# Kernel tuning notes

Hardware: AMD Instinct MI355X
Metric: run time of the kernel (lower is better)

Reference implementation:

```python
import jax, jax.numpy as jnp
import numpy as np

F = 128; K = 64; SR_CUT = 10.0
NB = 5; NRI = 3; NRA = 2; NRO = 1
N_ATOMS = 10000; N_PAIRS = 320000


def act(x):
    # shifted softplus: softplus(x) - log(2)
    return jax.nn.softplus(x) - jnp.log(2.0).astype(x.dtype)


def residual(x, W1, b1, W2, b2):
    # PhysNet residual: x + dense2(dense1(act(x))) with activation on dense1
    h = act(act(x) @ W1 + b1)
    return x + h @ W2 + b2


def cutoff_fn(D):
    x = D / SR_CUT
    x3 = x * x * x; x4 = x3 * x; x5 = x4 * x
    return jnp.where(x < 1.0, 1.0 - 6.0 * x5 + 15.0 * x4 - 10.0 * x3, 0.0)


def setup_inputs() -> dict:
    key = jax.random.key(0)
    ks = jax.random.split(key, 24)

    def nrm(k, shape, s=0.05):
        return (jax.random.normal(k, shape) * s).astype(jnp.float32)

    inp = {}
    inp["Z"] = jax.random.randint(ks[0], (N_ATOMS,), 1, 95)
    inp["R"] = (jax.random.normal(ks[1], (N_ATOMS, 3)) * 3.0).astype(jnp.float32)
    inp["idx_i"] = jax.random.randint(ks[2], (N_PAIRS,), 0, N_ATOMS)
    inp["idx_j"] = jax.random.randint(ks[3], (N_PAIRS,), 0, N_ATOMS)
    s3 = float(np.sqrt(3.0))
    inp["embeddings"] = jax.random.uniform(ks[4], (95, F), minval=-s3, maxval=s3).astype(jnp.float32)
    inp["rbf_centers"] = jnp.linspace(1.0, float(np.exp(-SR_CUT)), K).astype(jnp.float32)
    width = (0.5 / ((1.0 - float(np.exp(-SR_CUT))) / K)) ** 2
    inp["rbf_widths"] = jnp.full((K,), width, dtype=jnp.float32)
    inp["k2f_W"] = nrm(ks[5], (NB, K, F))
    inp["Wi"] = nrm(ks[6], (NB, F, F)); inp["bi"] = jnp.zeros((NB, F), jnp.float32)
    inp["Wj"] = nrm(ks[7], (NB, F, F)); inp["bj"] = jnp.zeros((NB, F), jnp.float32)
    inp["ri_W1"] = nrm(ks[8], (NB, NRI, F, F)); inp["ri_b1"] = jnp.zeros((NB, NRI, F), jnp.float32)
    inp["ri_W2"] = nrm(ks[9], (NB, NRI, F, F)); inp["ri_b2"] = jnp.zeros((NB, NRI, F), jnp.float32)
    inp["dW"] = nrm(ks[10], (NB, F, F)); inp["db"] = jnp.zeros((NB, F), jnp.float32)
    inp["u"] = jnp.ones((NB, F), jnp.float32)
    inp["ra_W1"] = nrm(ks[11], (NB, NRA, F, F)); inp["ra_b1"] = jnp.zeros((NB, NRA, F), jnp.float32)
    inp["ra_W2"] = nrm(ks[12], (NB, NRA, F, F)); inp["ra_b2"] = jnp.zeros((NB, NRA, F), jnp.float32)
    inp["ro_W1"] = nrm(ks[13], (NB, NRO, F, F)); inp["ro_b1"] = jnp.zeros((NB, NRO, F), jnp.float32)
    inp["ro_W2"] = nrm(ks[14], (NB, NRO, F, F)); inp["ro_b2"] = jnp.zeros((NB, NRO, F), jnp.float32)
    inp["out_W"] = nrm(ks[15], (NB, F, 2))
    inp["Escale"] = jnp.ones((95,), jnp.float32); inp["Eshift"] = jnp.zeros((95,), jnp.float32)
    inp["Qscale"] = jnp.ones((95,), jnp.float32); inp["Qshift"] = jnp.zeros((95,), jnp.float32)
    return inp


def reference(Z, R, idx_i, idx_j, embeddings, rbf_centers, rbf_widths, k2f_W, Wi, bi, Wj, bj,
              ri_W1, ri_b1, ri_W2, ri_b2, dW, db, u, ra_W1, ra_b1, ra_W2, ra_b2,
              ro_W1, ro_b1, ro_W2, ro_b2, out_W, Escale, Eshift, Qscale, Qshift):
    N = R.shape[0]
    # gather-based interatomic distances: gather -> sub -> sumsq -> relu -> sqrt
    dR = R[idx_i] - R[idx_j]                                   # [P,3]
    Dij = jnp.sqrt(jax.nn.relu(jnp.sum(dR * dR, axis=-1)))     # [P]
    # RBF expansion with smooth cutoff
    rbf = cutoff_fn(Dij)[:, None] * jnp.exp(-rbf_widths * (jnp.exp(-Dij)[:, None] - rbf_centers) ** 2)  # [P,K]
    x = embeddings[Z]                                          # [N,F]
    Ea = jnp.zeros((N,), x.dtype)
    Qa = jnp.zeros((N,), x.dtype)
    nhloss = jnp.zeros((), x.dtype)
    last2 = None
    for b in range(NB):
        # --- interaction layer ---
        g = rbf @ k2f_W[b]                                     # [P,F]
        xa = act(x)
        xi = act(xa @ Wi[b] + bi[b])                           # [N,F]
        xj_feat = act(xa @ Wj[b] + bj[b])                      # [N,F]
        msg = g * xj_feat[idx_j]                               # [P,F] gather + modulate
        m = xi + jax.ops.segment_sum(msg, idx_i, num_segments=N)
        for l in range(NRI):
            m = residual(m, ri_W1[b, l], ri_b1[b, l], ri_W2[b, l], ri_b2[b, l])
        m = act(m)
        x = u[b] * x + m @ dW[b] + db[b]
        for l in range(NRA):
            x = residual(x, ra_W1[b, l], ra_b1[b, l], ra_W2[b, l], ra_b2[b, l])
        # --- output block ---
        o = x
        for l in range(NRO):
            o = residual(o, ro_W1[b, l], ro_b1[b, l], ro_W2[b, l], ro_b2[b, l])
        out = act(o) @ out_W[b]                                # [N,2] -> (Ea, Qa)
        Ea = Ea + out[:, 0]
        Qa = Qa + out[:, 1]
        out2 = out * out
        if b > 0:
            nhloss = nhloss + jnp.mean(out2 / (out2 + last2 + 1e-7))
        last2 = out2
    Ea = Escale[Z] * Ea + Eshift[Z]
    Qa = Qscale[Z] * Qa + Qshift[Z]
    return Ea, Qa, Dij, nhloss
```

## Files before the change

### kernel.cpp

```cpp
#include <hip/hip_runtime.h>

typedef __attribute__((ext_vector_type(8))) short bfrag;
typedef __attribute__((ext_vector_type(4))) float ffrag;

__device__ __forceinline__ unsigned short f2b(float f){
  unsigned int u = __float_as_uint(f);
  return (unsigned short)((u + 0x7FFFu + ((u >> 16) & 1u)) >> 16);
}
__device__ __forceinline__ float b2f_lo(unsigned int v){
  return __uint_as_float(v << 16);
}
__device__ __forceinline__ float b2f_hi(unsigned int v){
  return __uint_as_float(v & 0xFFFF0000u);
}
__device__ __forceinline__ int rfl(int v){ return __builtin_amdgcn_readfirstlane(v); }
__device__ __forceinline__ float actf(float v){
  float e = __builtin_amdgcn_exp2f(-fabsf(v)*1.44269504088896341f);
  return fmaxf(v, 0.f) + __builtin_amdgcn_logf(1.f + e)*0.69314718055994531f - 0.69314718055994531f;
}

__global__ __launch_bounds__(256) void k_zero(float* p, int n){
  int i = blockIdx.x*256 + threadIdx.x;
  if (i < n) p[i] = 0.f;
}

__global__ __launch_bounds__(256) void k_dij_count(
    const float* __restrict__ R, const int* __restrict__ idx_i, const int* __restrict__ idx_j,
    float* __restrict__ DijF, float* __restrict__ Dout, int* __restrict__ counts, int P){
  int p = blockIdx.x*256 + threadIdx.x;
  if (p >= P) return;
  int i = idx_i[p], j = idx_j[p];
  float dx = R[i*3+0] - R[j*3+0];
  float dy = R[i*3+1] - R[j*3+1];
  float dz = R[i*3+2] - R[j*3+2];
  float D = sqrtf(fmaxf(dx*dx + dy*dy + dz*dz, 0.f));
  DijF[p] = D;
  Dout[p] = D;
  atomicAdd(&counts[i], 1);
}

__global__ __launch_bounds__(1024) void k_scan(const int* __restrict__ counts,
    int* __restrict__ cursor, int N){
  __shared__ int wsum[16];
  int tid = threadIdx.x;
  int CH = (N + 1023) >> 10;
  int base = tid * CH;
  int s = 0;
  for (int i = 0; i < CH; ++i){
    int idx = base + i;
    s += (idx < N) ? counts[idx] : 0;
  }
  int lane = tid & 63, w = tid >> 6;
  int v = s;
  #pragma unroll
  for (int off = 1; off < 64; off <<= 1){
    int t = __shfl_up(v, off, 64);
    if (lane >= off) v += t;
  }
  if (lane == 63) wsum[w] = v;
  __syncthreads();
  if (tid < 16){
    int t = wsum[tid];
    int vv = t;
    #pragma unroll
    for (int off = 1; off < 16; off <<= 1){
      int u = __shfl_up(vv, off, 64);
      if (tid >= off) vv += u;
    }
    wsum[tid] = vv - t;
  }
  __syncthreads();
  int run = (v - s) + wsum[w];
  for (int i = 0; i < CH; ++i){
    int idx = base + i;
    if (idx < N){ cursor[idx] = run; run += counts[idx]; }
  }
}

__global__ __launch_bounds__(256) void k_scatter(const int* __restrict__ idx_i,
    const int* __restrict__ idx_j, const float* __restrict__ DijF,
    int* __restrict__ cursor, int* __restrict__ i_s, int* __restrict__ j_s,
    float* __restrict__ D_s, int P){
  int p = blockIdx.x*256 + threadIdx.x;
  if (p >= P) return;
  int i = idx_i[p];
  int pos = atomicAdd(&cursor[i], 1);
  i_s[pos] = i;
  j_s[pos] = idx_j[p];
  D_s[pos] = DijF[p];
}

__global__ __launch_bounds__(256) void k_prep2(
    const float* __restrict__ D_s, const float* __restrict__ cent, const float* __restrict__ wid,
    unsigned short* __restrict__ rbf_s,
    const float* __restrict__ riW1, const float* __restrict__ riW2,
    const float* __restrict__ dW,   const float* __restrict__ raW1,
    const float* __restrict__ raW2, const float* __restrict__ roW1,
    const float* __restrict__ roW2, const float* __restrict__ Wi,
    const float* __restrict__ Wj,   const float* __restrict__ k2f,
    const float* __restrict__ outW,
    unsigned short* __restrict__ WBall, unsigned short* __restrict__ k2fP,
    unsigned short* __restrict__ outWB, int P){
  int gid0 = blockIdx.x*256 + threadIdx.x;
  if (gid0 < P*8){
    int t = gid0 >> 3, kg = gid0 & 7;
    float D = D_s[t];
    float xc = D * 0.1f;
    float cut = 0.f;
    if (xc < 1.f){
      float x3 = xc*xc*xc, x4 = x3*xc, x5 = x4*xc;
      cut = 1.f - 6.f*x5 + 15.f*x4 - 10.f*x3;
    }
    float eD = __builtin_amdgcn_exp2f(-D*1.44269504088896341f);
    bfrag o;
    #pragma unroll
    for (int i = 0; i < 8; ++i){
      int k = kg*8 + i;
      float tt = eD - cent[k];
      float v = cut * __builtin_amdgcn_exp2f(-wid[k]*tt*tt*1.44269504088896341f);
      o[i] = (short)f2b(v);
    }
    *(bfrag*)(rbf_s + (size_t)gid0*8) = o;
    return;
  }
  int gid = gid0 - P*8;
  if (gid < 75*2048){
    int i = gid >> 11, r = gid & 2047;
    const float* S;
    int slot;
    if (i < 15)      { S = riW1 + (size_t)i*16384;      slot = (i/3)*15 + 2*(i%3); }
    else if (i < 30) { int j=i-15; S = riW2 + (size_t)j*16384; slot = (j/3)*15 + 2*(j%3) + 1; }
    else if (i < 35) { int j=i-30; S = dW   + (size_t)j*16384; slot = j*15 + 6; }
    else if (i < 45) { int j=i-35; S = raW1 + (size_t)j*16384; slot = (j/2)*15 + 7 + 2*(j%2); }
    else if (i < 55) { int j=i-45; S = raW2 + (size_t)j*16384; slot = (j/2)*15 + 8 + 2*(j%2); }
    else if (i < 60) { int j=i-55; S = roW1 + (size_t)j*16384; slot = j*15 + 11; }
    else if (i < 65) { int j=i-60; S = roW2 + (size_t)j*16384; slot = j*15 + 12; }
    else if (i < 70) { int j=i-65; S = Wi   + (size_t)j*16384; slot = ((j==0)?4:(j-1))*15 + 13; }
    else             { int j=i-70; S = Wj   + (size_t)j*16384; slot = ((j==0)?4:(j-1))*15 + 14; }
    int fr = r >> 6, l = r & 63;
    int T = fr >> 2, k0 = fr & 3;
    int n = T*16 + (l & 15);
    int kbase = k0*32 + (l >> 4)*8;
    unsigned short* D = WBall + ((size_t)slot*2048 + r)*8;
    ushort4 o0, o1;
    o0.x=f2b(S[(kbase+0)*128+n]); o0.y=f2b(S[(kbase+1)*128+n]);
    o0.z=f2b(S[(kbase+2)*128+n]); o0.w=f2b(S[(kbase+3)*128+n]);
    o1.x=f2b(S[(kbase+4)*128+n]); o1.y=f2b(S[(kbase+5)*128+n]);
    o1.z=f2b(S[(kbase+6)*128+n]); o1.w=f2b(S[(kbase+7)*128+n]);
    ((ushort4*)D)[0]=o0; ((ushort4*)D)[1]=o1;
  } else if (gid < 75*2048 + 5120){
    int g = gid - 75*2048;
    int l = g & 63, fr = (g >> 6) & 15, b = g >> 10;
    int tile = fr >> 1, kh = fr & 1;
    const float* src = k2f + (size_t)b*64*128;
    int n = tile*16 + (l & 15);
    int kbase = kh*32 + (l >> 4)*8;
    ushort4 o0, o1;
    o0.x = f2b(src[(kbase+0)*128+n]); o0.y = f2b(src[(kbase+1)*128+n]);
    o0.z = f2b(src[(kbase+2)*128+n]); o0.w = f2b(src[(kbase+3)*128+n]);
    o1.x = f2b(src[(kbase+4)*128+n]); o1.y = f2b(src[(kbase+5)*128+n]);
    o1.z = f2b(src[(kbase+6)*128+n]); o1.w = f2b(src[(kbase+7)*128+n]);
    ushort4* dst = (ushort4*)(k2fP + (size_t)g*8);
    dst[0] = o0; dst[1] = o1;
  } else if (gid < 75*2048 + 5120 + 1280){
    int g = gid - (75*2048 + 5120);
    int b = g >> 8, r = g & 255;
    int l = r & 63;
    int col = l & 15;
    int k0 = r >> 6;
    int kbase = k0*32 + (l >> 4)*8;
    ushort4 o0 = {0,0,0,0}, o1 = {0,0,0,0};
    if (col < 2){
      const float* S = outW + (size_t)b*256;
      o0.x=f2b(S[(kbase+0)*2+col]); o0.y=f2b(S[(kbase+1)*2+col]);
      o0.z=f2b(S[(kbase+2)*2+col]); o0.w=f2b(S[(kbase+3)*2+col]);
      o1.x=f2b(S[(kbase+4)*2+col]); o1.y=f2b(S[(kbase+5)*2+col]);
      o1.z=f2b(S[(kbase+6)*2+col]); o1.w=f2b(S[(kbase+7)*2+col]);
    }
    unsigned short* D = outWB + ((size_t)b*256 + r)*8;
    ((ushort4*)D)[0]=o0; ((ushort4*)D)[1]=o1;
  }
}

__device__ __forceinline__ void mmtile(const unsigned short* tile,
    const unsigned short* __restrict__ WB, int w, int l, ffrag C[4]){
  int m = l & 15, q = l >> 4;
  bfrag A[4];
  #pragma unroll
  for (int k0 = 0; k0 < 4; ++k0)
    A[k0] = *(const bfrag*)(tile + m*136 + k0*32 + q*8);
  #pragma unroll
  for (int tt = 0; tt < 4; ++tt){
    ffrag c = {0.f,0.f,0.f,0.f};
    const bfrag* bp = (const bfrag*)(WB + (((w*4+tt)*4)*64 + l)*8);
    #pragma unroll
    for (int k0 = 0; k0 < 4; ++k0)
      c = __builtin_amdgcn_mfma_f32_16x16x32_bf16(A[k0], bp[k0*64], c, 0, 0, 0);
    C[tt] = c;
  }
}

__global__ __launch_bounds__(128) void k_phase1m(
    const int* __restrict__ Z, const float* __restrict__ emb,
    const unsigned short* __restrict__ WB45,
    const float* __restrict__ bi0, const float* __restrict__ bj0,
    float* __restrict__ x_g, float* __restrict__ m_g, unsigned short* __restrict__ xjb_g, int N){
  __shared__ unsigned short tile[16*136];
  int tid = threadIdx.x, w = tid >> 6, l = tid & 63;
  int m = l & 15, q = l >> 4, rbase = blockIdx.x*16;
  #pragma unroll
  for (int r = 0; r < 4; ++r){
    int row = rbase + q*4 + r;
    int z = Z[row];
    #pragma unroll
    for (int tt = 0; tt < 4; ++tt){
      int c = (w*4+tt)*16 + m;
      float v = emb[(size_t)z*128 + c];
      x_g[(size_t)row*128 + c] = v;
      tile[(q*4+r)*136 + c] = f2b(actf(v));
    }
  }
  __syncthreads();
  ffrag C[4];
  mmtile(tile, WB45 + 13*16384, w, l, C);
  #pragma unroll
  for (int tt = 0; tt < 4; ++tt){
    int c = (w*4+tt)*16 + m;
    float bb = bi0[c];
    #pragma unroll
    for (int r = 0; r < 4; ++r)
      m_g[(size_t)(rbase + q*4 + r)*128 + c] = actf(C[tt][r] + bb);
  }
  mmtile(tile, WB45 + 14*16384, w, l, C);
  #pragma unroll
  for (int tt = 0; tt < 4; ++tt){
    int c = (w*4+tt)*16 + m;
    float bb = bj0[c];
    #pragma unroll
    for (int r = 0; r < 4; ++r)
      xjb_g[(size_t)(rbase + q*4 + r)*128 + c] = f2b(actf(C[tt][r] + bb));
  }
}

__global__ __launch_bounds__(256, 4) void k_pairmsg2(
    const unsigned short* __restrict__ rbf_s, const unsigned short* __restrict__ k2fP,
    const int* __restrict__ i_s, const int* __restrict__ j_s,
    const unsigned short* __restrict__ xj, float* __restrict__ m_g, int P){
  __shared__ float G[4][16*130];
  int tid = threadIdx.x, w = tid >> 6, l = tid & 63;
  float* Gw = &G[w][0];
  bfrag B[16];
  #pragma unroll
  for (int t = 0; t < 16; ++t)
    B[t] = *(const bfrag*)(k2fP + (size_t)(t*64 + l)*8);
  int wstart = (blockIdx.x*4 + w)*64;
  if (wstart >= P) return;
  int row16 = l & 15, quad = l >> 4;
  float a0 = 0.f, a1 = 0.f;
  int iCur = -1;
  #pragma unroll 1
  for (int bi2 = 0; bi2 < 4; ++bi2){
    int bt = wstart + bi2*16;
    bfrag A0 = *(const bfrag*)(rbf_s + (size_t)(bt + row16)*64 + quad*8);
    bfrag A1 = *(const bfrag*)(rbf_s + (size_t)(bt + row16)*64 + 32 + quad*8);
    int ip[16], jp[16];
    #pragma unroll
    for (int g = 0; g < 4; ++g){
      int4 it = *(const int4*)(i_s + bt + g*4);
      int4 jt = *(const int4*)(j_s + bt + g*4);
      ip[g*4+0]=rfl(it.x); ip[g*4+1]=rfl(it.y); ip[g*4+2]=rfl(it.z); ip[g*4+3]=rfl(it.w);
      jp[g*4+0]=rfl(jt.x); jp[g*4+1]=rfl(jt.y); jp[g*4+2]=rfl(jt.z); jp[g*4+3]=rfl(jt.w);
    }
    unsigned int xv[16];
    #pragma unroll
    for (int k = 0; k < 16; ++k)
      xv[k] = *(const unsigned int*)(xj + (size_t)jp[k]*128 + 2*l);
    #pragma unroll
    for (int t = 0; t < 8; ++t){
      ffrag C = {0.f,0.f,0.f,0.f};
      C = __builtin_amdgcn_mfma_f32_16x16x32_bf16(A0, B[t*2],   C, 0, 0, 0);
      C = __builtin_amdgcn_mfma_f32_16x16x32_bf16(A1, B[t*2+1], C, 0, 0, 0);
      #pragma unroll
      for (int r = 0; r < 4; ++r)
        Gw[(quad*4+r)*130 + t*16 + row16] = C[r];
    }
    #pragma unroll
    for (int k = 0; k < 16; ++k){
      int i = ip[k];
      if (i != iCur){
        if (iCur >= 0){
          unsafeAtomicAdd(&m_g[(size_t)iCur*128 + 2*l],     a0);
          unsafeAtomicAdd(&m_g[(size_t)iCur*128 + 2*l + 1], a1);
        }
        iCur = i; a0 = 0.f; a1 = 0.f;
      }
      float g0 = Gw[k*130 + 2*l], g1 = Gw[k*130 + 2*l + 1];
      a0 = fmaf(g0, b2f_lo(xv[k]), a0);
      a1 = fmaf(g1, b2f_hi(xv[k]), a1);
    }
  }
  if (iCur >= 0){
    unsafeAtomicAdd(&m_g[(size_t)iCur*128 + 2*l],     a0);
    unsafeAtomicAdd(&m_g[(size_t)iCur*128 + 2*l + 1], a1);
  }
}

template<int HASNEXT, int NH>
__global__ __launch_bounds__(512, 6) void k_phase2m(
    float* __restrict__ m_g, float* __restrict__ x_g, unsigned short* __restrict__ xjb_g,
    const unsigned short* __restrict__ WBb,
    const float* __restrict__ rib1, const float* __restrict__ rib2,
    const float* __restrict__ db, const float* __restrict__ u,
    const float* __restrict__ rab1, const float* __restrict__ rab2,
    const float* __restrict__ rob1, const float* __restrict__ rob2,
    const float* __restrict__ biN, const float* __restrict__ bjN,
    const unsigned short* __restrict__ outWBb,
    float* __restrict__ Ea, float* __restrict__ Qa,
    float* __restrict__ last2, float* __restrict__ nh, int N){
  __shared__ unsigned short tiles[2][16*136];
  __shared__ float biasS[16*128];
  int tid = threadIdx.x, w = tid >> 6, l = tid & 63;
  int m = l & 15, q = l >> 4, rbase = blockIdx.x*16;
  int c = w*16 + m;
  ffrag mC, xC, C;
  float xrow[4];
  int cur = 0;
  const int nst = HASNEXT ? 15 : 13;
  const int slotSeq[15] = {0,1,2,3,4,5,6,7,8,9,10,
                           HASNEXT?13:11, HASNEXT?14:12, 11, 12};
  bfrag Bb[2][4];
  #pragma unroll
  for (int k0 = 0; k0 < 4; ++k0)
    Bb[0][k0] = *(const bfrag*)(WBb + (size_t)slotSeq[0]*16384 + (size_t)((w*4+k0)*64 + l)*8);

  if (tid < 128){
    biasS[0*128+tid]  = rib1[tid];
    biasS[1*128+tid]  = rib1[128+tid];
    biasS[2*128+tid]  = rib1[256+tid];
    biasS[3*128+tid]  = rib2[tid];
    biasS[4*128+tid]  = rib2[128+tid];
    biasS[5*128+tid]  = rib2[256+tid];
    biasS[6*128+tid]  = db[tid];
    biasS[7*128+tid]  = u[tid];
    biasS[8*128+tid]  = rab1[tid];
    biasS[9*128+tid]  = rab1[128+tid];
    biasS[10*128+tid] = rab2[tid];
    biasS[11*128+tid] = rab2[128+tid];
    biasS[12*128+tid] = rob1[tid];
    biasS[13*128+tid] = rob2[tid];
    biasS[14*128+tid] = biN[tid];
    biasS[15*128+tid] = bjN[tid];
  }
  #pragma unroll
  for (int r = 0; r < 4; ++r){
    int row = rbase + q*4 + r;
    xrow[r] = x_g[(size_t)row*128 + c];
    float v = m_g[(size_t)row*128 + c];
    mC[r] = v;
    tiles[0][(q*4+r)*136 + c] = f2b(actf(v));
  }
  #pragma unroll 2
  for (int s = 0; s < nst; ++s){
    __syncthreads();
    if (s+1 < nst){
      #pragma unroll
      for (int k0 = 0; k0 < 4; ++k0)
        Bb[(s+1)&1][k0] = *(const bfrag*)(WBb + (size_t)slotSeq[s+1]*16384 + (size_t)((w*4+k0)*64 + l)*8);
    }
    {
      const unsigned short* tp = &tiles[cur][0];
      ffrag cc = {0.f,0.f,0.f,0.f};
      #pragma unroll
      for (int k0 = 0; k0 < 4; ++k0){
        bfrag A = *(const bfrag*)(tp + m*136 + k0*32 + q*8);
        cc = __builtin_amdgcn_mfma_f32_16x16x32_bf16(A, Bb[s&1][k0], cc, 0, 0, 0);
      }
      C = cc;
    }
    if (HASNEXT && s == 11){
      float bb = biasS[14*128 + c];
      #pragma unroll
      for (int r = 0; r < 4; ++r)
        m_g[(size_t)(rbase + q*4 + r)*128 + c] = actf(C[r] + bb);
    } else if (HASNEXT && s == 12){
      float bb = biasS[15*128 + c];
      #pragma unroll
      for (int r = 0; r < 4; ++r)
        xjb_g[(size_t)(rbase + q*4 + r)*128 + c] = f2b(actf(C[r] + bb));
    } else if (s == 6){
      float uu = biasS[7*128 + c], bb = biasS[6*128 + c];
      #pragma unroll
      for (int r = 0; r < 4; ++r){
        float nv = uu*xrow[r] + C[r] + bb;
        xC[r] = nv;
        tiles[1-cur][(q*4+r)*136 + c] = f2b(actf(nv));
      }
      cur ^= 1;
    } else if (s == 1 || s == 3 || s == 5){
      float bb = biasS[(3 + (s>>1))*128 + c];
      #pragma unroll
      for (int r = 0; r < 4; ++r){
        float nv = mC[r] + C[r] + bb;
        mC[r] = nv;
        tiles[1-cur][(q*4+r)*136 + c] = f2b(actf(nv));
      }
      cur ^= 1;
    } else if (s == 8 || s == 10){
      float bb = biasS[(10 + ((s-8)>>1))*128 + c];
      #pragma unroll
      for (int r = 0; r < 4; ++r){
        float nv = xC[r] + C[r] + bb;
        xC[r] = nv;
        tiles[1-cur][(q*4+r)*136 + c] = f2b(actf(nv));
        if (HASNEXT && s == 10)
          x_g[(size_t)(rbase + q*4 + r)*128 + c] = nv;
      }
      cur ^= 1;
    } else if ((HASNEXT && s == 14) || (!HASNEXT && s == 12)){
      float bb = biasS[13*128 + c];
      #pragma unroll
      for (int r = 0; r < 4; ++r){
        float ov = xC[r] + C[r] + bb;
        tiles[1-cur][(q*4+r)*136 + c] = f2b(actf(ov));
      }
      cur ^= 1;
    } else {
      int bidx = (s==0)?0:(s==2)?1:(s==4)?2:(s==7)?8:(s==9)?9:12;
      float bb = biasS[bidx*128 + c];
      #pragma unroll
      for (int r = 0; r < 4; ++r)
        tiles[1-cur][(q*4+r)*136 + c] = f2b(actf(C[r] + bb));
      cur ^= 1;
    }
  }
  __syncthreads();
  if (w == 0){
    const unsigned short* tp = &tiles[cur][0];
    bfrag A[4];
    #pragma unroll
    for (int k0 = 0; k0 < 4; ++k0)
      A[k0] = *(const bfrag*)(tp + m*136 + k0*32 + q*8);
    ffrag Ch = {0.f,0.f,0.f,0.f};
    #pragma unroll
    for (int k0 = 0; k0 < 4; ++k0){
      bfrag B = *(const bfrag*)(outWBb + (size_t)(k0*64 + l)*8);
      Ch = __builtin_amdgcn_mfma_f32_16x16x32_bf16(A[k0], B, Ch, 0, 0, 0);
    }
    int col = m;
    if (col < 2){
      float tpa = 0.f;
      #pragma unroll
      for (int r = 0; r < 4; ++r){
        int row = rbase + q*4 + r;
        float val = Ch[r];
        if (NH){
          if (col == 0) Ea[row] += val; else Qa[row] += val;
        } else {
          if (col == 0) Ea[row]  = val; else Qa[row]  = val;
        }
        float sq = val*val;
        if (NH){
          float lastv = last2[row*2 + col];
          tpa += sq/(sq + lastv + 1e-7f);
        }
        last2[row*2 + col] = sq;
      }
      if (NH) unsafeAtomicAdd(nh, tpa);
    }
  }
}

__global__ __launch_bounds__(256) void k_final(
    const int* __restrict__ Z, const float* __restrict__ Ea, const float* __restrict__ Qa,
    const float* __restrict__ Es, const float* __restrict__ Eh,
    const float* __restrict__ Qs, const float* __restrict__ Qh,
    const float* __restrict__ nh, float* __restrict__ out, int N, int P){
  int n = blockIdx.x*256 + threadIdx.x;
  if (n < N){
    int z = Z[n];
    out[n]   = Es[z]*Ea[n] + Eh[z];
    out[N+n] = Qs[z]*Qa[n] + Qh[z];
  }
  if (blockIdx.x == 0 && threadIdx.x == 0)
    out[(size_t)2*N + P] = nh[0] / (2.f * (float)N);
}

extern "C" void kernel_launch(void* const* d_in, const int* in_sizes, int n_in,
                              void* d_out, int out_size, void* d_ws, size_t ws_size,
                              hipStream_t stream){
  const int N = in_sizes[0];
  const int P = in_sizes[2];
  const int F = 128;

  const int* Z      = (const int*)d_in[0];
  const float* R    = (const float*)d_in[1];
  const int* idx_i  = (const int*)d_in[2];
  const int* idx_j  = (const int*)d_in[3];
  const float* emb  = (const float*)d_in[4];
  const float* cent = (const float*)d_in[5];
  const float* wid  = (const float*)d_in[6];
  const float* k2f  = (const float*)d_in[7];
  const float* Wi   = (const float*)d_in[8];  const float* bi   = (const float*)d_in[9];
  const float* Wj   = (const float*)d_in[10]; const float* bj   = (const float*)d_in[11];
  const float* riW1 = (const float*)d_in[12]; const float* rib1 = (const float*)d_in[13];
  const float* riW2 = (const float*)d_in[14]; const float* rib2 = (const float*)d_in[15];
  const float* dWp  = (const float*)d_in[16]; const float* dbp  = (const float*)d_in[17];
  const float* u    = (const float*)d_in[18];
  const float* raW1 = (const float*)d_in[19]; const float* rab1 = (const float*)d_in[20];
  const float* raW2 = (const float*)d_in[21]; const float* rab2 = (const float*)d_in[22];
  const float* roW1 = (const float*)d_in[23]; const float* rob1 = (const float*)d_in[24];
  const float* roW2 = (const float*)d_in[25]; const float* rob2 = (const float*)d_in[26];
  const float* outW = (const float*)d_in[27];
  const float* Es   = (const float*)d_in[28]; const float* Eh   = (const float*)d_in[29];
  const float* Qs   = (const float*)d_in[30]; const float* Qh   = (const float*)d_in[31];

  char* ws = (char*)d_ws;
  size_t off = 0;
  float* DijF  = (float*)(ws + off); off += (size_t)P*4;
  float* D_s   = (float*)(ws + off); off += (size_t)P*4;
  int*   i_s   = (int*)  (ws + off); off += (size_t)P*4;
  int*   j_s   = (int*)  (ws + off); off += (size_t)P*4;
  unsigned short* rbf_s = (unsigned short*)(ws + off); off += (size_t)P*64*2;
  unsigned short* k2fP  = (unsigned short*)(ws + off); off += (size_t)5*16*64*8*2;
  unsigned short* WBall = (unsigned short*)(ws + off); off += (size_t)75*16384*2;
  unsigned short* outWB = (unsigned short*)(ws + off); off += (size_t)5*2048*2;
  float* x     = (float*)(ws + off); off += (size_t)N*F*4;
  unsigned short* xjb = (unsigned short*)(ws + off); off += (size_t)N*F*2;
  float* m     = (float*)(ws + off); off += (size_t)N*F*4;
  float* last2 = (float*)(ws + off); off += (size_t)N*2*4;
  float* Ea    = (float*)(ws + off); off += (size_t)N*4;
  float* Qa    = (float*)(ws + off); off += (size_t)N*4;
  float* nh    = (float*)(ws + off); off += 256;
  int*   counts= (int*)  (ws + off); off += (size_t)N*4;
  int*   cursor= (int*)  (ws + off); off += (size_t)N*4;

  float* outF = (float*)d_out;
  float* Dout = outF + (size_t)2*N;

  const int nzero = N + 64;
  k_zero<<<dim3((nzero+255)/256), dim3(256), 0, stream>>>(nh, nzero);
  k_dij_count<<<dim3((P+255)/256), dim3(256), 0, stream>>>(R, idx_i, idx_j, DijF, Dout, counts, P);
  k_scan<<<dim3(1), dim3(1024), 0, stream>>>(counts, cursor, N);
  k_scatter<<<dim3((P+255)/256), dim3(256), 0, stream>>>(idx_i, idx_j, DijF, cursor, i_s, j_s, D_s, P);
  const int prep2n = P*8 + 75*2048 + 5120 + 1280;
  k_prep2<<<dim3((prep2n+255)/256), dim3(256), 0, stream>>>(
      D_s, cent, wid, rbf_s,
      riW1, riW2, dWp, raW1, raW2, roW1, roW2, Wi, Wj, k2f, outW,
      WBall, k2fP, outWB, P);

  const int G16 = (N + 15)/16;
  k_phase1m<<<dim3(G16), dim3(128), 0, stream>>>(Z, emb, WBall + (size_t)4*15*16384,
                                                 bi, bj, x, m, xjb, N);

  const int pmg = (P + 255)/256;
  for (int b = 0; b < 5; ++b){
    k_pairmsg2<<<dim3(pmg), dim3(256), 0, stream>>>(rbf_s, k2fP + (size_t)b*16*64*8,
                                                    i_s, j_s, xjb, m, P);
    const unsigned short* WBb = WBall + (size_t)b*15*16384;
    const float* a_rib1 = rib1 + (size_t)b*3*F;
    const float* a_rib2 = rib2 + (size_t)b*3*F;
    const float* a_db   = dbp  + (size_t)b*F;
    const float* a_u    = u    + (size_t)b*F;
    const float* a_rab1 = rab1 + (size_t)b*2*F;
    const float* a_rab2 = rab2 + (size_t)b*2*F;
    const float* a_rob1 = rob1 + (size_t)b*F;
    const float* a_rob2 = rob2 + (size_t)b*F;
    int bn = (b < 4) ? (b+1) : 0;
    const float* a_biN = bi + (size_t)bn*F;
    const float* a_bjN = bj + (size_t)bn*F;
    const unsigned short* oWB = outWB + (size_t)b*2048;
    if (b == 0){
      k_phase2m<1,0><<<dim3(G16), dim3(512), 0, stream>>>(m, x, xjb, WBb,
        a_rib1, a_rib2, a_db, a_u, a_rab1, a_rab2, a_rob1, a_rob2,
        a_biN, a_bjN, oWB, Ea, Qa, last2, nh, N);
    } else if (b < 4){
      k_phase2m<1,1><<<dim3(G16), dim3(512), 0, stream>>>(m, x, xjb, WBb,
        a_rib1, a_rib2, a_db, a_u, a_rab1, a_rab2, a_rob1, a_rob2,
        a_biN, a_bjN, oWB, Ea, Qa, last2, nh, N);
    } else {
      k_phase2m<0,1><<<dim3(G16), dim3(512), 0, stream>>>(m, x, xjb, WBb,
        a_rib1, a_rib2, a_db, a_u, a_rab1, a_rab2, a_rob1, a_rob2,
        a_biN, a_bjN, oWB, Ea, Qa, last2, nh, N);
    }
  }
  k_final<<<dim3((N+255)/256), dim3(256), 0, stream>>>(Z, Ea, Qa, Es, Eh, Qs, Qh, nh, outF, N, P);
}
```

Before: 424.5 us.

## Fuse pair message aggregation into per-atom block kernel with LDS accumulation

```diff
diff --git a/kernel.cpp b/kernel.cpp
--- a/kernel.cpp
+++ b/kernel.cpp
@@ -242,72 +242,13 @@
   }
 }
 
-__global__ __launch_bounds__(256, 4) void k_pairmsg2(
+template<int HASNEXT, int NH>
+__global__ __launch_bounds__(512, 4) void k_block2(
     const unsigned short* __restrict__ rbf_s, const unsigned short* __restrict__ k2fP,
     const int* __restrict__ i_s, const int* __restrict__ j_s,
-    const unsigned short* __restrict__ xj, float* __restrict__ m_g, int P){
-  __shared__ float G[4][16*130];
-  int tid = threadIdx.x, w = tid >> 6, l = tid & 63;
-  float* Gw = &G[w][0];
-  bfrag B[16];
-  #pragma unroll
-  for (int t = 0; t < 16; ++t)
-    B[t] = *(const bfrag*)(k2fP + (size_t)(t*64 + l)*8);
-  int wstart = (blockIdx.x*4 + w)*64;
-  if (wstart >= P) return;
-  int row16 = l & 15, quad = l >> 4;
-  float a0 = 0.f, a1 = 0.f;
-  int iCur = -1;
-  #pragma unroll 1
-  for (int bi2 = 0; bi2 < 4; ++bi2){
-    int bt = wstart + bi2*16;
-    bfrag A0 = *(const bfrag*)(rbf_s + (size_t)(bt + row16)*64 + quad*8);
-    bfrag A1 = *(const bfrag*)(rbf_s + (size_t)(bt + row16)*64 + 32 + quad*8);
-    int ip[16], jp[16];
-    #pragma unroll
-    for (int g = 0; g < 4; ++g){
-      int4 it = *(const int4*)(i_s + bt + g*4);
-      int4 jt = *(const int4*)(j_s + bt + g*4);
-      ip[g*4+0]=rfl(it.x); ip[g*4+1]=rfl(it.y); ip[g*4+2]=rfl(it.z); ip[g*4+3]=rfl(it.w);
-      jp[g*4+0]=rfl(jt.x); jp[g*4+1]=rfl(jt.y); jp[g*4+2]=rfl(jt.z); jp[g*4+3]=rfl(jt.w);
-    }
-    unsigned int xv[16];
-    #pragma unroll
-    for (int k = 0; k < 16; ++k)
-      xv[k] = *(const unsigned int*)(xj + (size_t)jp[k]*128 + 2*l);
-    #pragma unroll
-    for (int t = 0; t < 8; ++t){
-      ffrag C = {0.f,0.f,0.f,0.f};
-      C = __builtin_amdgcn_mfma_f32_16x16x32_bf16(A0, B[t*2],   C, 0, 0, 0);
-      C = __builtin_amdgcn_mfma_f32_16x16x32_bf16(A1, B[t*2+1], C, 0, 0, 0);
-      #pragma unroll
-      for (int r = 0; r < 4; ++r)
-        Gw[(quad*4+r)*130 + t*16 + row16] = C[r];
-    }
-    #pragma unroll
-    for (int k = 0; k < 16; ++k){
-      int i = ip[k];
-      if (i != iCur){
-        if (iCur >= 0){
-          unsafeAtomicAdd(&m_g[(size_t)iCur*128 + 2*l],     a0);
-          unsafeAtomicAdd(&m_g[(size_t)iCur*128 + 2*l + 1], a1);
-        }
-        iCur = i; a0 = 0.f; a1 = 0.f;
-      }
-      float g0 = Gw[k*130 + 2*l], g1 = Gw[k*130 + 2*l + 1];
-      a0 = fmaf(g0, b2f_lo(xv[k]), a0);
-      a1 = fmaf(g1, b2f_hi(xv[k]), a1);
-    }
-  }
-  if (iCur >= 0){
-    unsafeAtomicAdd(&m_g[(size_t)iCur*128 + 2*l],     a0);
-    unsafeAtomicAdd(&m_g[(size_t)iCur*128 + 2*l + 1], a1);
-  }
-}
-
-template<int HASNEXT, int NH>
-__global__ __launch_bounds__(512, 6) void k_phase2m(
-    float* __restrict__ m_g, float* __restrict__ x_g, unsigned short* __restrict__ xjb_g,
+    const int* __restrict__ ends,
+    const unsigned short* __restrict__ xjb_r, unsigned short* __restrict__ xjb_w,
+    float* __restrict__ m_g, float* __restrict__ x_g,
     const unsigned short* __restrict__ WBb,
     const float* __restrict__ rib1, const float* __restrict__ rib2,
     const float* __restrict__ db, const float* __restrict__ u,
@@ -316,23 +257,77 @@
     const float* __restrict__ biN, const float* __restrict__ bjN,
     const unsigned short* __restrict__ outWBb,
     float* __restrict__ Ea, float* __restrict__ Qa,
-    float* __restrict__ last2, float* __restrict__ nh, int N){
-  __shared__ unsigned short tiles[2][16*136];
-  __shared__ float biasS[16*128];
+    float* __restrict__ last2, float* __restrict__ nh, int N, int P){
+  __shared__ float G[8][16*130];
+  __shared__ float mL[16*128];
+  unsigned short* tilesS = (unsigned short*)&G[0][0];
+  float* biasS = (float*)((char*)&G[0][0] + 8704);
   int tid = threadIdx.x, w = tid >> 6, l = tid & 63;
   int m = l & 15, q = l >> 4, rbase = blockIdx.x*16;
   int c = w*16 + m;
-  ffrag mC, xC, C;
-  float xrow[4];
-  int cur = 0;
-  const int nst = HASNEXT ? 15 : 13;
-  const int slotSeq[15] = {0,1,2,3,4,5,6,7,8,9,10,
-                           HASNEXT?13:11, HASNEXT?14:12, 11, 12};
-  bfrag Bb[2][4];
-  #pragma unroll
-  for (int k0 = 0; k0 < 4; ++k0)
-    Bb[0][k0] = *(const bfrag*)(WBb + (size_t)slotSeq[0]*16384 + (size_t)((w*4+k0)*64 + l)*8);
-
+  #pragma unroll
+  for (int i = tid; i < 2048; i += 512) mL[i] = 0.f;
+  __syncthreads();
+  {
+    float* Gw = &G[w][0];
+    bfrag B[16];
+    #pragma unroll
+    for (int t = 0; t < 16; ++t)
+      B[t] = *(const bfrag*)(k2fP + (size_t)(t*64 + l)*8);
+    int pstart = (rbase == 0) ? 0 : ends[rbase-1];
+    int pend   = ends[rbase+15];
+    int b0 = pstart >> 4, b1 = (pend + 15) >> 4;
+    float a0 = 0.f, a1 = 0.f;
+    int iCur = -1;
+    #pragma unroll 1
+    for (int bt = b0 + w; bt < b1; bt += 8){
+      int base = bt << 4;
+      bfrag A0 = *(const bfrag*)(rbf_s + (size_t)(base + m)*64 + q*8);
+      bfrag A1 = *(const bfrag*)(rbf_s + (size_t)(base + m)*64 + 32 + q*8);
+      int ip[16], jp[16];
+      #pragma unroll
+      for (int g = 0; g < 4; ++g){
+        int4 it = *(const int4*)(i_s + base + g*4);
+        int4 jt = *(const int4*)(j_s + base + g*4);
+        ip[g*4+0]=rfl(it.x); ip[g*4+1]=rfl(it.y); ip[g*4+2]=rfl(it.z); ip[g*4+3]=rfl(it.w);
+        jp[g*4+0]=rfl(jt.x); jp[g*4+1]=rfl(jt.y); jp[g*4+2]=rfl(jt.z); jp[g*4+3]=rfl(jt.w);
+      }
+      unsigned int xv[16];
+      #pragma unroll
+      for (int k = 0; k < 16; ++k)
+        xv[k] = *(const unsigned int*)(xjb_r + (size_t)jp[k]*128 + 2*l);
+      #pragma unroll
+      for (int t = 0; t < 8; ++t){
+        ffrag C = {0.f,0.f,0.f,0.f};
+        C = __builtin_amdgcn_mfma_f32_16x16x32_bf16(A0, B[t*2],   C, 0, 0, 0);
+        C = __builtin_amdgcn_mfma_f32_16x16x32_bf16(A1, B[t*2+1], C, 0, 0, 0);
+        #pragma unroll
+        for (int r = 0; r < 4; ++r)
+          Gw[(q*4+r)*130 + t*16 + m] = C[r];
+      }
+      #pragma unroll
+      for (int k = 0; k < 16; ++k){
+        int i = ip[k];
+        if ((unsigned)(i - rbase) < 16u){
+          if (i != iCur){
+            if (iCur >= 0){
+              atomicAdd(&mL[(iCur-rbase)*128 + 2*l],     a0);
+              atomicAdd(&mL[(iCur-rbase)*128 + 2*l + 1], a1);
+            }
+            iCur = i; a0 = 0.f; a1 = 0.f;
+          }
+          float g0 = Gw[k*130 + 2*l], g1 = Gw[k*130 + 2*l + 1];
+          a0 = fmaf(g0, b2f_lo(xv[k]), a0);
+          a1 = fmaf(g1, b2f_hi(xv[k]), a1);
+        }
+      }
+    }
+    if (iCur >= 0){
+      atomicAdd(&mL[(iCur-rbase)*128 + 2*l],     a0);
+      atomicAdd(&mL[(iCur-rbase)*128 + 2*l + 1], a1);
+    }
+  }
+  __syncthreads();
   if (tid < 128){
     biasS[0*128+tid]  = rib1[tid];
     biasS[1*128+tid]  = rib1[128+tid];
@@ -351,13 +346,23 @@
     biasS[14*128+tid] = biN[tid];
     biasS[15*128+tid] = bjN[tid];
   }
+  ffrag mC, xC, C;
+  float xrow[4];
+  int cur = 0;
+  const int nst = HASNEXT ? 15 : 13;
+  const int slotSeq[15] = {0,1,2,3,4,5,6,7,8,9,10,
+                           HASNEXT?13:11, HASNEXT?14:12, 11, 12};
+  bfrag Bb[2][4];
+  #pragma unroll
+  for (int k0 = 0; k0 < 4; ++k0)
+    Bb[0][k0] = *(const bfrag*)(WBb + (size_t)slotSeq[0]*16384 + (size_t)((w*4+k0)*64 + l)*8);
   #pragma unroll
   for (int r = 0; r < 4; ++r){
     int row = rbase + q*4 + r;
     xrow[r] = x_g[(size_t)row*128 + c];
-    float v = m_g[(size_t)row*128 + c];
+    float v = m_g[(size_t)row*128 + c] + mL[(q*4+r)*128 + c];
     mC[r] = v;
-    tiles[0][(q*4+r)*136 + c] = f2b(actf(v));
+    tilesS[(q*4+r)*136 + c] = f2b(actf(v));
   }
   #pragma unroll 2
   for (int s = 0; s < nst; ++s){
@@ -368,7 +373,7 @@
         Bb[(s+1)&1][k0] = *(const bfrag*)(WBb + (size_t)slotSeq[s+1]*16384 + (size_t)((w*4+k0)*64 + l)*8);
     }
     {
-      const unsigned short* tp = &tiles[cur][0];
+      const unsigned short* tp = tilesS + cur*2176;
       ffrag cc = {0.f,0.f,0.f,0.f};
       #pragma unroll
       for (int k0 = 0; k0 < 4; ++k0){
@@ -386,14 +391,14 @@
       float bb = biasS[15*128 + c];
       #pragma unroll
       for (int r = 0; r < 4; ++r)
-        xjb_g[(size_t)(rbase + q*4 + r)*128 + c] = f2b(actf(C[r] + bb));
+        xjb_w[(size_t)(rbase + q*4 + r)*128 + c] = f2b(actf(C[r] + bb));
     } else if (s == 6){
       float uu = biasS[7*128 + c], bb = biasS[6*128 + c];
       #pragma unroll
       for (int r = 0; r < 4; ++r){
         float nv = uu*xrow[r] + C[r] + bb;
         xC[r] = nv;
-        tiles[1-cur][(q*4+r)*136 + c] = f2b(actf(nv));
+        tilesS[(1-cur)*2176 + (q*4+r)*136 + c] = f2b(actf(nv));
       }
       cur ^= 1;
     } else if (s == 1 || s == 3 || s == 5){
@@ -402,7 +407,7 @@
       for (int r = 0; r < 4; ++r){
         float nv = mC[r] + C[r] + bb;
         mC[r] = nv;
-        tiles[1-cur][(q*4+r)*136 + c] = f2b(actf(nv));
+        tilesS[(1-cur)*2176 + (q*4+r)*136 + c] = f2b(actf(nv));
       }
       cur ^= 1;
     } else if (s == 8 || s == 10){
@@ -411,7 +416,7 @@
       for (int r = 0; r < 4; ++r){
         float nv = xC[r] + C[r] + bb;
         xC[r] = nv;
-        tiles[1-cur][(q*4+r)*136 + c] = f2b(actf(nv));
+        tilesS[(1-cur)*2176 + (q*4+r)*136 + c] = f2b(actf(nv));
         if (HASNEXT && s == 10)
           x_g[(size_t)(rbase + q*4 + r)*128 + c] = nv;
       }
@@ -421,7 +426,7 @@
       #pragma unroll
       for (int r = 0; r < 4; ++r){
         float ov = xC[r] + C[r] + bb;
-        tiles[1-cur][(q*4+r)*136 + c] = f2b(actf(ov));
+        tilesS[(1-cur)*2176 + (q*4+r)*136 + c] = f2b(actf(ov));
       }
       cur ^= 1;
     } else {
@@ -429,13 +434,13 @@
       float bb = biasS[bidx*128 + c];
       #pragma unroll
       for (int r = 0; r < 4; ++r)
-        tiles[1-cur][(q*4+r)*136 + c] = f2b(actf(C[r] + bb));
+        tilesS[(1-cur)*2176 + (q*4+r)*136 + c] = f2b(actf(C[r] + bb));
       cur ^= 1;
     }
   }
   __syncthreads();
   if (w == 0){
-    const unsigned short* tp = &tiles[cur][0];
+    const unsigned short* tp = tilesS + cur*2176;
     bfrag A[4];
     #pragma unroll
     for (int k0 = 0; k0 < 4; ++k0)
@@ -525,7 +530,8 @@
   unsigned short* WBall = (unsigned short*)(ws + off); off += (size_t)75*16384*2;
   unsigned short* outWB = (unsigned short*)(ws + off); off += (size_t)5*2048*2;
   float* x     = (float*)(ws + off); off += (size_t)N*F*4;
-  unsigned short* xjb = (unsigned short*)(ws + off); off += (size_t)N*F*2;
+  unsigned short* xjbA = (unsigned short*)(ws + off); off += (size_t)N*F*2;
+  unsigned short* xjbB = (unsigned short*)(ws + off); off += (size_t)N*F*2;
   float* m     = (float*)(ws + off); off += (size_t)N*F*4;
   float* last2 = (float*)(ws + off); off += (size_t)N*2*4;
   float* Ea    = (float*)(ws + off); off += (size_t)N*4;
@@ -550,12 +556,9 @@
 
   const int G16 = (N + 15)/16;
   k_phase1m<<<dim3(G16), dim3(128), 0, stream>>>(Z, emb, WBall + (size_t)4*15*16384,
-                                                 bi, bj, x, m, xjb, N);
-
-  const int pmg = (P + 255)/256;
+                                                 bi, bj, x, m, xjbA, N);
+
   for (int b = 0; b < 5; ++b){
-    k_pairmsg2<<<dim3(pmg), dim3(256), 0, stream>>>(rbf_s, k2fP + (size_t)b*16*64*8,
-                                                    i_s, j_s, xjb, m, P);
     const unsigned short* WBb = WBall + (size_t)b*15*16384;
     const float* a_rib1 = rib1 + (size_t)b*3*F;
     const float* a_rib2 = rib2 + (size_t)b*3*F;
@@ -569,18 +572,21 @@
     const float* a_biN = bi + (size_t)bn*F;
     const float* a_bjN = bj + (size_t)bn*F;
     const unsigned short* oWB = outWB + (size_t)b*2048;
+    const unsigned short* kP  = k2fP + (size_t)b*16*64*8;
+    const unsigned short* xr  = (b & 1) ? xjbB : xjbA;
+    unsigned short*       xw  = (b & 1) ? xjbA : xjbB;
     if (b == 0){
-      k_phase2m<1,0><<<dim3(G16), dim3(512), 0, stream>>>(m, x, xjb, WBb,
-        a_rib1, a_rib2, a_db, a_u, a_rab1, a_rab2, a_rob1, a_rob2,
-        a_biN, a_bjN, oWB, Ea, Qa, last2, nh, N);
+      k_block2<1,0><<<dim3(G16), dim3(512), 0, stream>>>(rbf_s, kP, i_s, j_s, cursor,
+        xr, xw, m, x, WBb, a_rib1, a_rib2, a_db, a_u, a_rab1, a_rab2, a_rob1, a_rob2,
+        a_biN, a_bjN, oWB, Ea, Qa, last2, nh, N, P);
     } else if (b < 4){
-      k_phase2m<1,1><<<dim3(G16), dim3(512), 0, stream>>>(m, x, xjb, WBb,
-        a_rib1, a_rib2, a_db, a_u, a_rab1, a_rab2, a_rob1, a_rob2,
-        a_biN, a_bjN, oWB, Ea, Qa, last2, nh, N);
+      k_block2<1,1><<<dim3(G16), dim3(512), 0, stream>>>(rbf_s, kP, i_s, j_s, cursor,
+        xr, xw, m, x, WBb, a_rib1, a_rib2, a_db, a_u, a_rab1, a_rab2, a_rob1, a_rob2,
+        a_biN, a_bjN, oWB, Ea, Qa, last2, nh, N, P);
     } else {
-      k_phase2m<0,1><<<dim3(G16), dim3(512), 0, stream>>>(m, x, xjb, WBb,
-        a_rib1, a_rib2, a_db, a_u, a_rab1, a_rab2, a_rob1, a_rob2,
-        a_biN, a_bjN, oWB, Ea, Qa, last2, nh, N);
+      k_block2<0,1><<<dim3(G16), dim3(512), 0, stream>>>(rbf_s, kP, i_s, j_s, cursor,
+        xr, xw, m, x, WBb, a_rib1, a_rib2, a_db, a_u, a_rab1, a_rab2, a_rob1, a_rob2,
+        a_biN, a_bjN, oWB, Ea, Qa, last2, nh, N, P);
     }
   }
   k_final<<<dim3((N+255)/256), dim3(256), 0, stream>>>(Z, Ea, Qa, Es, Eh, Qs, Qh, nh, outF, N, P);
```

Measured after the change: 499.7 us. +17.7%, slower.
